# Optimization experiments

Measured on AMD Instinct MI355X. Metric: run time of the kernel, lower is better.

## Reference

```python
import jax, jax.numpy as jnp
import numpy as np

NUM_EMBEDDINGS = 1024
EMBEDDING_DIM = 256
COMMITMENT_COST = 0.25


def setup_inputs() -> dict:
    key = jax.random.key(0)
    k_z, k_e = jax.random.split(key)
    z = jax.random.normal(k_z, (8, EMBEDDING_DIM, 16, 16, 16), dtype=jnp.float32)
    # nn.Embedding weight initialized uniform(-1/K, 1/K)
    codebook = jax.random.uniform(
        k_e, (NUM_EMBEDDINGS, EMBEDDING_DIM), dtype=jnp.float32,
        minval=-1.0 / NUM_EMBEDDINGS, maxval=1.0 / NUM_EMBEDDINGS)
    return {"z": z, "codebook": codebook}


def reference(z, codebook):
    B, D, H, W, L = z.shape
    # (B, D, H, W, L) -> (B, H, W, L, D) -> (N, D)
    z_perm = jnp.transpose(z, (0, 2, 3, 4, 1))          # (B,H,W,L,D)
    z_flat = z_perm.reshape(-1, D)                       # (N,D)
    # squared-distance via expansion: ||z||^2 + ||e||^2 - 2 z.e^T
    distances = ((z_flat ** 2).sum(axis=1, keepdims=True)
                 + (codebook ** 2).sum(axis=1)
                 - 2.0 * z_flat @ codebook.T)            # (N,K)
    indices = jnp.argmin(distances, axis=1)              # (N,)
    quantized = codebook[indices].reshape(B, H, W, L, D)
    idx_out = indices.reshape(B, H, W, L)
    # losses (stop_gradient mirrors .detach())
    e_latent_loss = jnp.mean((jax.lax.stop_gradient(quantized) - z_perm) ** 2)
    q_latent_loss = jnp.mean((quantized - jax.lax.stop_gradient(z_perm)) ** 2)
    vq_loss = q_latent_loss + COMMITMENT_COST * e_latent_loss
    # straight-through estimator
    quant_st = z_perm + jax.lax.stop_gradient(quantized - z_perm)
    quant_out = jnp.transpose(quant_st, (0, 4, 1, 2, 3))  # (B,D,H,W,L)
    return quant_out, idx_out, vq_loss
```

## Files before the change

### kernel.cpp

```cpp
#include <hip/hip_runtime.h>


#define K_CODES 1024
#define DIM 256
#define N_TOK 32768
#define SPATIAL 4096
#define TOK_BLK 64
#define NBLK (N_TOK / TOK_BLK)
#define CAP 28
#define MARGIN 1e-3f

typedef __attribute__((ext_vector_type(8))) short short8;
typedef __attribute__((ext_vector_type(4))) float float4v;

#define WS_LOSS 0
#define WS_CNT 8
#define WS_E2 16
#define WS_EB 2048

#define O_IDX (8 * DIM * SPATIAL)
#define O_LOSS (O_IDX + N_TOK)

__device__ __forceinline__ short f2bf(float v) {
  unsigned u = __float_as_uint(v);
  u = (u + 0x7fffu + ((u >> 16) & 1u)) >> 16;
  return (short)u;
}

__global__ __launch_bounds__(256) void prep_kernel(const float* __restrict__ e,
                                                   float* __restrict__ ws) {
  __shared__ float sq[DIM];
  __shared__ __align__(16) short sbf[DIM];
  __shared__ float chv[16];
  int k = blockIdx.x, d = threadIdx.x;
  float v = e[k * DIM + d];
  sbf[d] = f2bf(v);
  sq[d] = __fmul_rn(v, v);
  __syncthreads();
  if (d < 32) {
    int f = d >> 2, q = d & 3;
    int stage = k >> 6, ct = (k >> 4) & 3, nn = k & 15;
    short8 chunk = *(const short8*)(sbf + f * 32 + q * 8);
    int off8 = ((stage * 4 + ct) * 8 + f) * 64 + q * 16 + nn;
    ((short8*)(ws + WS_EB))[off8] = chunk;
  }
  if (d < 16) {
    int blkb = d >> 3, j = d & 7;
    const float* x = sq + blkb * 128;
    float c = x[j];
#pragma unroll
    for (int i = 1; i < 16; i++) c = __fadd_rn(c, x[i * 8 + j]);
    chv[d] = c;
  }
  __syncthreads();
  if (d == 0) {
    float a0 = __fadd_rn(__fadd_rn(chv[0], chv[1]), __fadd_rn(chv[2], chv[3]));
    float a1 = __fadd_rn(__fadd_rn(chv[4], chv[5]), __fadd_rn(chv[6], chv[7]));
    float resA = __fadd_rn(a0, a1);
    float b0 = __fadd_rn(__fadd_rn(chv[8], chv[9]), __fadd_rn(chv[10], chv[11]));
    float b1 = __fadd_rn(__fadd_rn(chv[12], chv[13]), __fadd_rn(chv[14], chv[15]));
    float resB = __fadd_rn(b0, b1);
    ws[WS_E2 + k] = __fadd_rn(resA, resB);
    if (k == 0) {
      ws[WS_LOSS] = 0.f;
      ((unsigned*)ws)[WS_CNT] = 0u;
    }
  }
}

__global__ __launch_bounds__(512, 4) void main_kernel(const float* __restrict__ z,
                                                      const float* __restrict__ e,
                                                      float* __restrict__ ws,
                                                      float* __restrict__ out) {
  __shared__ __align__(16) short Bst[64 * 256];
  __shared__ unsigned short cand[TOK_BLK][CAP];
  __shared__ float cands[TOK_BLK][CAP];
  __shared__ float aminv[2][TOK_BLK];
  __shared__ int cnt[TOK_BLK];
  __shared__ float Szp[2][TOK_BLK];
  __shared__ int mini_sh[TOK_BLK];
  __shared__ float red[8];

  int tid = threadIdx.x, w = tid >> 6, lane = tid & 63;
  int quad = lane >> 4, nn = lane & 15;
  int g = w & 3, kh = w >> 2;
  int n0 = blockIdx.x * TOK_BLK;
  int b = n0 >> 12, s0 = n0 & 4095;
  const float* zb = z + (size_t)b * DIM * SPATIAL + s0;
  const float* Se = ws + WS_E2;
  const uint4* eBg = (const uint4*)(ws + WS_EB);
  if (tid < TOK_BLK) cnt[tid] = 0;

  {
    const float* zp = zb + g * 16 + nn;
    float r0, r1;
    {
      int j0 = quad * 2;
      float v0 = zp[(size_t)(kh * 128 + j0) * SPATIAL];
      float v1 = zp[(size_t)(kh * 128 + j0 + 1) * SPATIAL];
      r0 = __fmul_rn(v0, v0);
      r1 = __fmul_rn(v1, v1);
      for (int i = 1; i < 16; i++) {
        v0 = zp[(size_t)(kh * 128 + i * 8 + j0) * SPATIAL];
        v1 = zp[(size_t)(kh * 128 + i * 8 + j0 + 1) * SPATIAL];
        r0 = __fadd_rn(r0, __fmul_rn(v0, v0));
        r1 = __fadd_rn(r1, __fmul_rn(v1, v1));
      }
    }
    float p = __fadd_rn(r0, r1);
    float s1 = __fadd_rn(p, __shfl_xor(p, 16));
    float s2 = __fadd_rn(s1, __shfl_xor(s1, 32));
    if (quad == 0) Szp[kh][g * 16 + nn] = s2;
  }

  int tokA = g * 16 + nn;
  short8 A[8];
#pragma unroll
  for (int f = 0; f < 8; f++) {
    short8 a;
#pragma unroll
    for (int j = 0; j < 8; j++) {
      int d = f * 32 + quad * 8 + j;
      a[j] = f2bf(zb[(size_t)d * SPATIAL + tokA]);
    }
    A[f] = a;
  }

  float thr[4] = {3.4e38f, 3.4e38f, 3.4e38f, 3.4e38f};
  for (int stage = 0; stage < 16; stage++) {
    __syncthreads();
#pragma unroll
    for (int i = 0; i < 4; i++)
      ((uint4*)Bst)[i * 512 + tid] = eBg[(size_t)stage * 2048 + i * 512 + tid];
    __syncthreads();

    for (int ctl = 0; ctl < 2; ctl++) {
      int ct = kh * 2 + ctl;
      int kbase = stage * 64 + ct * 16;
      float4v C = {0.f, 0.f, 0.f, 0.f};
      const short8* Bp = (const short8*)Bst + ct * 8 * 64;
#pragma unroll
      for (int f = 0; f < 8; f++) {
        short8 Bf = Bp[f * 64 + lane];
        C = __builtin_amdgcn_mfma_f32_16x16x32_bf16(A[f], Bf, C, 0, 0, 0);
      }
      float SeK = Se[kbase + nn];
      float sv[4];
      bool pr[4];
#pragma unroll
      for (int r = 0; r < 4; r++) {
        float s = fmaf(-2.f, C[r], SeK);
        float m = s;
        m = fminf(m, __shfl_xor(m, 1, 16));
        m = fminf(m, __shfl_xor(m, 2, 16));
        m = fminf(m, __shfl_xor(m, 4, 16));
        m = fminf(m, __shfl_xor(m, 8, 16));
        thr[r] = fminf(thr[r], m);
        sv[r] = s;
        pr[r] = s < thr[r] + MARGIN;
      }
      if (__ballot(pr[0] | pr[1] | pr[2] | pr[3])) {
#pragma unroll
        for (int r = 0; r < 4; r++) {
          unsigned long long bl = __ballot(pr[r]);
          unsigned grp = (unsigned)((bl >> (quad * 16)) & 0xffffULL);
          if (grp) {
            int tb = g * 16 + quad * 4 + r;
            int base = 0;
            if (nn == 0) base = atomicAdd(&cnt[tb], __popc(grp));
            base = __shfl(base, quad * 16);
            if (pr[r]) {
              int pos = base + __popc(grp & ((1u << nn) - 1u));
              if (pos < CAP) {
                cand[tb][pos] = (unsigned short)(kbase + nn);
                cands[tb][pos] = sv[r];
              }
            }
          }
        }
      }
    }
  }
#pragma unroll
  for (int r = 0; r < 4; r++)
    if (nn == 0) aminv[kh][g * 16 + quad * 4 + r] = thr[r];
  __syncthreads();

  int tl = lane >> 3, oct = lane & 7;
  int tb = w * 8 + tl;
  int cc = cnt[tb];
  int cl = cc < CAP ? cc : CAP;
  float bestD = 3.4e38f;
  int bestk = 0x7fffffff;
  float SznT = __fadd_rn(Szp[0][tb], Szp[1][tb]);
  {
    const float* zp = zb + tb;
    float amin = fminf(aminv[0][tb], aminv[1][tb]);
    for (int c = oct; c < cl; c += 8) {
      if (cands[tb][c] >= amin + MARGIN) continue;
      int k = cand[tb][c];
      const float* er = e + (size_t)k * DIM;
      float acc = 0.f;
#pragma unroll 4
      for (int dd = 0; dd < DIM; dd += 4) {
        float4 e4 = *(const float4*)(er + dd);
        acc = fmaf(zp[(size_t)(dd + 0) * SPATIAL], e4.x, acc);
        acc = fmaf(zp[(size_t)(dd + 1) * SPATIAL], e4.y, acc);
        acc = fmaf(zp[(size_t)(dd + 2) * SPATIAL], e4.z, acc);
        acc = fmaf(zp[(size_t)(dd + 3) * SPATIAL], e4.w, acc);
      }
      float D = __fsub_rn(__fadd_rn(SznT, Se[k]), __fmul_rn(2.f, acc));
      if (D < bestD || (D == bestD && k < bestk)) { bestD = D; bestk = k; }
    }
  }
#pragma unroll
  for (int off = 4; off >= 1; off >>= 1) {
    float oD = __shfl_down(bestD, off, 8);
    int ok = __shfl_down(bestk, off, 8);
    if (oD < bestD || (oD == bestD && ok < bestk)) { bestD = oD; bestk = ok; }
  }
  if (oct == 0 && cc <= CAP) {
    mini_sh[tb] = bestk;
    out[O_IDX + n0 + tb] = (float)bestk;
  }
  for (int t = 0; t < 8; t++) {
    int tb2 = w * 8 + t;
    if (cnt[tb2] > CAP) {
      const float* zq = zb + tb2;
      float Szn = __fadd_rn(Szp[0][tb2], Szp[1][tb2]);
      float bD = 3.4e38f;
      int bk = 0x7fffffff;
      for (int k = lane; k < K_CODES; k += 64) {
        const float* er = e + (size_t)k * DIM;
        float acc = 0.f;
#pragma unroll 4
        for (int dd = 0; dd < DIM; dd += 4) {
          float4 e4 = *(const float4*)(er + dd);
          acc = fmaf(zq[(size_t)(dd + 0) * SPATIAL], e4.x, acc);
          acc = fmaf(zq[(size_t)(dd + 1) * SPATIAL], e4.y, acc);
          acc = fmaf(zq[(size_t)(dd + 2) * SPATIAL], e4.z, acc);
          acc = fmaf(zq[(size_t)(dd + 3) * SPATIAL], e4.w, acc);
        }
        float D = __fsub_rn(__fadd_rn(Szn, Se[k]), __fmul_rn(2.f, acc));
        if (D < bD || (D == bD && k < bk)) { bD = D; bk = k; }
      }
#pragma unroll
      for (int m = 1; m < 64; m <<= 1) {
        float oD = __shfl_xor(bD, m);
        int ok = __shfl_xor(bk, m);
        if (oD < bD || (oD == bD && ok < bk)) { bD = oD; bk = ok; }
      }
      if (lane == 0) {
        mini_sh[tb2] = bk;
        out[O_IDX + n0 + tb2] = (float)bk;
      }
    }
  }
  __syncthreads();

  int mten = mini_sh[lane];
  const float* erow = e + (size_t)mten * DIM;
  float* op = out + (size_t)b * DIM * SPATIAL + s0;
  float sumsq = 0.f;
#pragma unroll 2
  for (int i4 = 0; i4 < 32; i4 += 4) {
    int d = w * 32 + i4;
    float4 v4 = *(const float4*)(erow + d);
#pragma unroll
    for (int m = 0; m < 4; m++) {
      float v = (m == 0) ? v4.x : (m == 1) ? v4.y : (m == 2) ? v4.z : v4.w;
      float zv = zb[(size_t)(d + m) * SPATIAL + lane];
      float df = __fsub_rn(v, zv);
      sumsq = fmaf(df, df, sumsq);
      op[(size_t)(d + m) * SPATIAL + lane] = v;
    }
  }
#pragma unroll
  for (int o = 32; o > 0; o >>= 1) sumsq += __shfl_down(sumsq, o, 64);
  if (lane == 0) red[w] = sumsq;
  __syncthreads();
  if (tid == 0) {
    float rs = ((red[0] + red[1]) + (red[2] + red[3])) +
               ((red[4] + red[5]) + (red[6] + red[7]));
    atomicAdd(ws + WS_LOSS, rs);
    __threadfence();
    unsigned t = atomicAdd((unsigned*)ws + WS_CNT, 1u);
    if (t == NBLK - 1) {
      float total = atomicAdd(ws + WS_LOSS, 0.f);
      out[O_LOSS] = 1.25f * total / 8388608.f;
    }
  }
}

extern "C" void kernel_launch(void* const* d_in, const int* in_sizes, int n_in,
                              void* d_out, int out_size, void* d_ws, size_t ws_size,
                              hipStream_t stream) {
  const float* z = (const float*)d_in[0];
  const float* e = (const float*)d_in[1];
  float* ws = (float*)d_ws;
  float* out = (float*)d_out;

  prep_kernel<<<K_CODES, 256, 0, stream>>>(e, ws);
  main_kernel<<<NBLK, 512, 0, stream>>>(z, e, ws, out);
}
```

Baseline: 203.4 us.

## Stage z tile once in padded shared memory and reuse across all phases

Loads the block's 64-token by 256-dim z tile from global memory once with coalesced float4 reads, transposes it into a padded LDS buffer, and uses that buffer for the norm computation, the bf16 A-fragment build, the candidate rescoring, the fallback search and the loss pass. This replaces repeated strided global reads of z (stride SPATIAL) in each phase. The extra ~66KB of shared memory lowers occupancy, and launch bounds drop from 4 to 2 blocks per CU to match.

```diff
diff --git a/kernel.cpp b/kernel.cpp
--- a/kernel.cpp
+++ b/kernel.cpp
@@ -9,6 +9,7 @@
 #define NBLK (N_TOK / TOK_BLK)
 #define CAP 28
 #define MARGIN 1e-3f
+#define ZLD 257
 
 typedef __attribute__((ext_vector_type(8))) short short8;
 typedef __attribute__((ext_vector_type(4))) float float4v;
@@ -68,11 +69,12 @@
   }
 }
 
-__global__ __launch_bounds__(512, 4) void main_kernel(const float* __restrict__ z,
+__global__ __launch_bounds__(512, 2) void main_kernel(const float* __restrict__ z,
                                                       const float* __restrict__ e,
                                                       float* __restrict__ ws,
                                                       float* __restrict__ out) {
   __shared__ __align__(16) short Bst[64 * 256];
+  __shared__ float zt[TOK_BLK * ZLD];
   __shared__ unsigned short cand[TOK_BLK][CAP];
   __shared__ float cands[TOK_BLK][CAP];
   __shared__ float aminv[2][TOK_BLK];
@@ -91,18 +93,30 @@
   const uint4* eBg = (const uint4*)(ws + WS_EB);
   if (tid < TOK_BLK) cnt[tid] = 0;
 
+#pragma unroll
+  for (int it = 0; it < 8; it++) {
+    int c = it * 512 + tid;
+    int d = c >> 4, t4 = (c & 15) << 2;
+    float4 v4 = *(const float4*)(zb + (size_t)d * SPATIAL + t4);
+    zt[(t4 + 0) * ZLD + d] = v4.x;
+    zt[(t4 + 1) * ZLD + d] = v4.y;
+    zt[(t4 + 2) * ZLD + d] = v4.z;
+    zt[(t4 + 3) * ZLD + d] = v4.w;
+  }
+  __syncthreads();
+
   {
-    const float* zp = zb + g * 16 + nn;
+    const float* zp = zt + (g * 16 + nn) * ZLD + kh * 128;
     float r0, r1;
     {
       int j0 = quad * 2;
-      float v0 = zp[(size_t)(kh * 128 + j0) * SPATIAL];
-      float v1 = zp[(size_t)(kh * 128 + j0 + 1) * SPATIAL];
+      float v0 = zp[j0];
+      float v1 = zp[j0 + 1];
       r0 = __fmul_rn(v0, v0);
       r1 = __fmul_rn(v1, v1);
       for (int i = 1; i < 16; i++) {
-        v0 = zp[(size_t)(kh * 128 + i * 8 + j0) * SPATIAL];
-        v1 = zp[(size_t)(kh * 128 + i * 8 + j0 + 1) * SPATIAL];
+        v0 = zp[i * 8 + j0];
+        v1 = zp[i * 8 + j0 + 1];
         r0 = __fadd_rn(r0, __fmul_rn(v0, v0));
         r1 = __fadd_rn(r1, __fmul_rn(v1, v1));
       }
@@ -113,16 +127,13 @@
     if (quad == 0) Szp[kh][g * 16 + nn] = s2;
   }
 
-  int tokA = g * 16 + nn;
+  const float* zrowA = zt + (g * 16 + nn) * ZLD;
   short8 A[8];
 #pragma unroll
   for (int f = 0; f < 8; f++) {
     short8 a;
 #pragma unroll
-    for (int j = 0; j < 8; j++) {
-      int d = f * 32 + quad * 8 + j;
-      a[j] = f2bf(zb[(size_t)d * SPATIAL + tokA]);
-    }
+    for (int j = 0; j < 8; j++) a[j] = f2bf(zrowA[f * 32 + quad * 8 + j]);
     A[f] = a;
   }
 
@@ -194,7 +205,7 @@
   int bestk = 0x7fffffff;
   float SznT = __fadd_rn(Szp[0][tb], Szp[1][tb]);
   {
-    const float* zp = zb + tb;
+    const float* zp = zt + tb * ZLD;
     float amin = fminf(aminv[0][tb], aminv[1][tb]);
     for (int c = oct; c < cl; c += 8) {
       if (cands[tb][c] >= amin + MARGIN) continue;
@@ -204,10 +215,10 @@
 #pragma unroll 4
       for (int dd = 0; dd < DIM; dd += 4) {
         float4 e4 = *(const float4*)(er + dd);
-        acc = fmaf(zp[(size_t)(dd + 0) * SPATIAL], e4.x, acc);
-        acc = fmaf(zp[(size_t)(dd + 1) * SPATIAL], e4.y, acc);
-        acc = fmaf(zp[(size_t)(dd + 2) * SPATIAL], e4.z, acc);
-        acc = fmaf(zp[(size_t)(dd + 3) * SPATIAL], e4.w, acc);
+        acc = fmaf(zp[dd + 0], e4.x, acc);
+        acc = fmaf(zp[dd + 1], e4.y, acc);
+        acc = fmaf(zp[dd + 2], e4.z, acc);
+        acc = fmaf(zp[dd + 3], e4.w, acc);
       }
       float D = __fsub_rn(__fadd_rn(SznT, Se[k]), __fmul_rn(2.f, acc));
       if (D < bestD || (D == bestD && k < bestk)) { bestD = D; bestk = k; }
@@ -226,7 +237,7 @@
   for (int t = 0; t < 8; t++) {
     int tb2 = w * 8 + t;
     if (cnt[tb2] > CAP) {
-      const float* zq = zb + tb2;
+      const float* zq = zt + tb2 * ZLD;
       float Szn = __fadd_rn(Szp[0][tb2], Szp[1][tb2]);
       float bD = 3.4e38f;
       int bk = 0x7fffffff;
@@ -236,10 +247,10 @@
 #pragma unroll 4
         for (int dd = 0; dd < DIM; dd += 4) {
           float4 e4 = *(const float4*)(er + dd);
-          acc = fmaf(zq[(size_t)(dd + 0) * SPATIAL], e4.x, acc);
-          acc = fmaf(zq[(size_t)(dd + 1) * SPATIAL], e4.y, acc);
-          acc = fmaf(zq[(size_t)(dd + 2) * SPATIAL], e4.z, acc);
-          acc = fmaf(zq[(size_t)(dd + 3) * SPATIAL], e4.w, acc);
+          acc = fmaf(zq[dd + 0], e4.x, acc);
+          acc = fmaf(zq[dd + 1], e4.y, acc);
+          acc = fmaf(zq[dd + 2], e4.z, acc);
+          acc = fmaf(zq[dd + 3], e4.w, acc);
         }
         float D = __fsub_rn(__fadd_rn(Szn, Se[k]), __fmul_rn(2.f, acc));
         if (D < bD || (D == bD && k < bk)) { bD = D; bk = k; }
@@ -260,6 +271,7 @@
 
   int mten = mini_sh[lane];
   const float* erow = e + (size_t)mten * DIM;
+  const float* zrow = zt + lane * ZLD;
   float* op = out + (size_t)b * DIM * SPATIAL + s0;
   float sumsq = 0.f;
 #pragma unroll 2
@@ -269,7 +281,7 @@
 #pragma unroll
     for (int m = 0; m < 4; m++) {
       float v = (m == 0) ? v4.x : (m == 1) ? v4.y : (m == 2) ? v4.z : v4.w;
-      float zv = zb[(size_t)(d + m) * SPATIAL + lane];
+      float zv = zrow[d + m];
       float df = __fsub_rn(v, zv);
       sumsq = fmaf(df, df, sumsq);
       op[(size_t)(d + m) * SPATIAL + lane] = v;
```

After: 207.8 us. 2.2% more time.
